# Optimization experiments

Hardware: AMD Instinct MI355X
Metric: run time of the kernel (lower is better)

Reference implementation:

```python
import jax, jax.numpy as jnp
import numpy as np

NUM_TRAIN = 256  # num_train_anchors
N, A, T = 8, 131072, 64


def _make_boxes(key, shape2):
    # shape2 = (..., 2) of (y, x); returns valid boxes (y1, x1, y2, x2) in [0, 1]
    k1, k2 = jax.random.split(key)
    c1 = jax.random.uniform(k1, shape2, dtype=jnp.float32)
    c2 = jax.random.uniform(k2, shape2, dtype=jnp.float32)
    lo = jnp.minimum(c1, c2)
    hi = jnp.maximum(c1, c2)
    return jnp.stack([lo[..., 0], lo[..., 1], hi[..., 0], hi[..., 1]], axis=-1)


def setup_inputs() -> dict:
    key = jax.random.key(0)
    ka, kt, kp, kn = jax.random.split(key, 4)
    return {
        "anchors": _make_boxes(ka, (N, A, 2)),
        "true_bboxes": _make_boxes(kt, (N, T, 2)),
        "rand_pos": jax.random.uniform(kp, (N, A), dtype=jnp.float32),
        "rand_neg": jax.random.uniform(kn, (N, A), dtype=jnp.float32),
    }


def _bbox_overlap(anchors, gt):
    # anchors [A,4], gt [T,4] -> IoU [A,T]
    ay1, ax1, ay2, ax2 = [anchors[:, i] for i in range(4)]
    gy1, gx1, gy2, gx2 = [gt[:, i] for i in range(4)]
    a_area = (ay2 - ay1) * (ax2 - ax1)                       # [A]
    g_area = (gy2 - gy1) * (gx2 - gx1)                       # [T]
    ih = jnp.clip(jnp.minimum(ay2[:, None], gy2[None, :]) - jnp.maximum(ay1[:, None], gy1[None, :]), 0.0)
    iw = jnp.clip(jnp.minimum(ax2[:, None], gx2[None, :]) - jnp.maximum(ax1[:, None], gx1[None, :]), 0.0)
    inter = ih * iw                                          # [A,T]
    union = a_area[:, None] + g_area[None, :] - inter
    return jnp.where(union > 0, inter / jnp.where(union > 0, union, 1.0), 0.0)


def _rank_of(scores):
    # rank[i] = position of element i in ascending sort of scores
    order = jnp.argsort(scores)
    return jnp.zeros(scores.shape[0], jnp.int32).at[order].set(jnp.arange(scores.shape[0], dtype=jnp.int32))


def _compute_bbox_deltas(anchors, gt):
    # standard (dy, dx, dh, dw) encoding with safe denominators
    ah = anchors[:, 2] - anchors[:, 0]
    aw = anchors[:, 3] - anchors[:, 1]
    acy = anchors[:, 0] + 0.5 * ah
    acx = anchors[:, 1] + 0.5 * aw
    gh = gt[:, 2] - gt[:, 0]
    gw = gt[:, 3] - gt[:, 1]
    gcy = gt[:, 0] + 0.5 * gh
    gcx = gt[:, 1] + 0.5 * gw
    ah_s = jnp.where(ah > 0, ah, 1.0)
    aw_s = jnp.where(aw > 0, aw, 1.0)
    gh_s = jnp.where(gh > 0, gh, 1.0)
    gw_s = jnp.where(gw > 0, gw, 1.0)
    return jnp.stack([(gcy - acy) / ah_s, (gcx - acx) / aw_s,
                      jnp.log(gh_s / ah_s), jnp.log(gw_s / aw_s)], axis=-1)


def _get_targets(anchors, gt, r_pos, r_neg):
    na = anchors.shape[0]
    # strip_out_of_bounds_anchors: zero out anchors falling outside [0,1]^2 (keeps static shape)
    inb = (anchors[:, 0] >= 0) & (anchors[:, 1] >= 0) & (anchors[:, 2] <= 1) & (anchors[:, 3] <= 1)
    anchors = jnp.where(inb[:, None], anchors, 0.0)

    overlaps = _bbox_overlap(anchors, gt)                    # [A,T]

    # --- class assignment ---
    iou_max_val = jnp.max(overlaps, axis=1)                  # [A]
    classes = jnp.full((na,), -1, jnp.int32)
    classes = jnp.where(iou_max_val < 0.3, 0, classes)
    iou_max_anchor = jnp.argmax(overlaps, axis=0)            # [T] best anchor per gt
    pos_anchor = jnp.zeros((na,), jnp.int32).at[iou_max_anchor].set(1)
    classes = jnp.where(pos_anchor > 0, 1, classes)
    classes = jnp.where(iou_max_val >= 0.7, 1, classes)

    # --- subsample positives to NUM_TRAIN//2 (uniform random subset) ---
    pos = classes > 0
    rank_p = _rank_of(jnp.where(pos, r_pos, jnp.inf))
    keep_pos = pos & (rank_p < NUM_TRAIN // 2)
    classes = jnp.where(pos & ~keep_pos, -1, classes)
    n_pos = jnp.sum(keep_pos.astype(jnp.int32))

    # --- subsample negatives to NUM_TRAIN - n_pos ---
    desired_neg = NUM_TRAIN - n_pos
    neg = classes == 0
    rank_n = _rank_of(jnp.where(neg, r_neg, jnp.inf))
    keep_neg = neg & (rank_n < desired_neg)
    classes = jnp.where(neg & ~keep_neg, -1, classes)

    # --- deltas for positive anchors ---
    best_gt = jnp.argmax(overlaps, axis=1)                   # [A]
    deltas = _compute_bbox_deltas(anchors, gt[best_gt])      # [A,4]
    deltas = jnp.where((classes > 0)[:, None], deltas, 0.0)
    return classes, deltas


def reference(anchors, true_bboxes, rand_pos, rand_neg):
    classes, deltas = jax.vmap(_get_targets)(anchors, true_bboxes, rand_pos, rand_neg)
    return classes, deltas
```

## Files before the change

kernel.cpp:

```cpp
#include <hip/hip_runtime.h>
#include <stdint.h>

#define N_B 8
#define A_N 131072
#define T_N 64
#define NUM_TRAIN 256
#define NEG_TAU 0.05f
#define ITEM_CAP 512
#define HSET 512
#define APT 4
#define SEG_A 1024
#define GBLK_A 128
#define CAPP 128
#define KB_THREADS 1024
#define BLK_C 128
#define SEG_C 1024

typedef unsigned long long u64;
typedef unsigned int u32;

__device__ __forceinline__ float iou_one(float ay1, float ax1, float ay2, float ax2,
                                         float a_area, float gy1, float gx1, float gy2,
                                         float gx2, float g_area) {
#pragma clang fp contract(off)
    float ih = fmaxf(fminf(ay2, gy2) - fmaxf(ay1, gy1), 0.0f);
    float iw = fmaxf(fminf(ax2, gx2) - fmaxf(ax1, gx1), 0.0f);
    float inter = ih * iw;
    float uni = (a_area + g_area) - inter;
    return uni > 0.0f ? inter / uni : 0.0f;
}

__global__ void __launch_bounds__(256) k_main(const float4* __restrict__ anchors4,
                                              const float4* __restrict__ gts4,
                                              const float* __restrict__ rpos,
                                              const float* __restrict__ rneg,
                                              unsigned char* __restrict__ preclass,
                                              long long* __restrict__ colpack,
                                              u64* __restrict__ pos_list,
                                              u64* __restrict__ neg_list,
                                              int* __restrict__ bcp, int* __restrict__ bcn,
                                              int* __restrict__ hist_pos,
                                              int* __restrict__ hist_neg) {
    __shared__ float4 gbox[T_N];
    __shared__ float gars[T_N];
    __shared__ u64 cmax[T_N];
    __shared__ int lcnt[2];
    int n = blockIdx.y, bx = blockIdx.x, tid = threadIdx.x, lane = tid & 63;
    int a0 = bx * SEG_A + tid;
    size_t nA = (size_t)n * A_N;

    if (tid < T_N) {
        float4 gb = gts4[n * T_N + tid];
        gbox[tid] = gb;
        {
#pragma clang fp contract(off)
            gars[tid] = (gb.z - gb.x) * (gb.w - gb.y);
        }
        cmax[tid] = 0;
    }
    if (tid < 2) lcnt[tid] = 0;
    __syncthreads();

    float ay1[APT], ax1[APT], ay2[APT], ax2[APT], aar[APT], vmax[APT];
#pragma unroll
    for (int k = 0; k < APT; k++) {
        float4 ab = anchors4[nA + a0 + k * 256];
        float y1 = ab.x, x1 = ab.y, y2 = ab.z, x2 = ab.w;
        bool inb = (y1 >= 0.f) && (x1 >= 0.f) && (y2 <= 1.f) && (x2 <= 1.f);
        if (!inb) { y1 = x1 = y2 = x2 = 0.f; }
        ay1[k] = y1; ax1[k] = x1; ay2[k] = y2; ax2[k] = x2;
        {
#pragma clang fp contract(off)
            aar[k] = (y2 - y1) * (x2 - x1);
        }
        vmax[k] = 0.f;
    }

#pragma unroll 4
    for (int jj = 0; jj < T_N; jj++) {
        int j = (lane + jj) & (T_N - 1);
        float4 gb = gbox[j];
        float gar = gars[j];
        float vb = iou_one(ay1[0], ax1[0], ay2[0], ax2[0], aar[0], gb.x, gb.y, gb.z, gb.w, gar);
        vmax[0] = fmaxf(vmax[0], vb);
        int kb = 0;
#pragma unroll
        for (int k = 1; k < APT; k++) {
            float v = iou_one(ay1[k], ax1[k], ay2[k], ax2[k], aar[k], gb.x, gb.y, gb.z, gb.w, gar);
            vmax[k] = fmaxf(vmax[k], v);
            if (v > vb) { vb = v; kb = k; }
        }
        u64 pk = ((u64)__float_as_uint(vb) << 32) | (u32)(~(u32)(a0 + (kb << 8)));
        atomicMax(&cmax[j], pk);
    }

    size_t segbase = ((size_t)(n * GBLK_A + bx)) << 7;
#pragma unroll
    for (int k = 0; k < APT; k++) {
        int a = a0 + k * 256;
        float vm = vmax[k];
        int c0 = (vm < 0.3f) ? 0 : ((vm >= 0.7f) ? 1 : -1);
        preclass[nA + a] = (unsigned char)(signed char)c0;
        if (c0 == 1) {
            int sl = atomicAdd(&lcnt[0], 1);
            if (sl < CAPP) {
                float r = rpos[nA + a];
                pos_list[segbase + sl] = ((u64)__float_as_uint(r) << 32) | (u32)a;
                int bb = (int)(r * 256.0f); bb = bb > 255 ? 255 : bb;
                atomicAdd(&hist_pos[(n << 8) + bb], 1);
            }
        } else if (c0 == 0) {
            float r = rneg[nA + a];
            if (r < NEG_TAU) {
                int sl = atomicAdd(&lcnt[1], 1);
                if (sl < CAPP) {
                    neg_list[segbase + sl] = ((u64)__float_as_uint(r) << 32) | (u32)a;
                    int bb = (int)(r * (256.0f / NEG_TAU)); bb = bb > 255 ? 255 : bb;
                    atomicAdd(&hist_neg[(n << 8) + bb], 1);
                }
            }
        }
    }
    __syncthreads();
    if (tid < T_N) atomicMax(&colpack[(n << 6) + tid], (long long)cmax[tid]);
    if (tid == 0) {
        bcp[n * GBLK_A + bx] = lcnt[0] < CAPP ? lcnt[0] : CAPP;
        bcn[n * GBLK_A + bx] = lcnt[1] < CAPP ? lcnt[1] : CAPP;
    }
}

__device__ __forceinline__ bool in_hset(const int* hset, int a) {
    u32 h = ((u32)a * 2654435761u) >> 23 & (HSET - 1);
    while (true) {
        int v = hset[h];
        if (v == -1) return false;
        if (v == a) return true;
        h = (h + 1) & (HSET - 1);
    }
}

__device__ u64 select_from_hist(const u64* lists, const int* cnts,
                                const u64* extras, int ecnt, const int* hset, bool use_excl,
                                int k, float scale, u64 ovf_all,
                                int* hist, u64* items, int* misc, int* wsum, u64* result) {
    int tid = threadIdx.x, lane = tid & 63, wid = tid >> 6;
    if (tid == 0) { misc[0] = 0; *result = ovf_all; }
    __syncthreads();

    int h = 0, v = 0;
    if (tid < 256) { h = hist[tid]; v = h; }
#pragma unroll
    for (int d = 1; d < 64; d <<= 1) {
        int t = __shfl_up(v, d, 64);
        if (lane >= d) v += t;
    }
    if (tid < 256 && lane == 63) wsum[wid] = v;
    __syncthreads();
    int total = wsum[0] + wsum[1] + wsum[2] + wsum[3];
    if (tid < 256) {
        int base = 0;
        for (int w = 0; w < wid; w++) base += wsum[w];
        int incl = base + v, exc = incl - h;
        if (k >= exc && k < incl) { misc[1] = tid; misc[2] = exc; }
    }
    __syncthreads();
    if (k >= total) return ovf_all;
    int b = misc[1], before = misc[2];

    int seg = tid & (GBLK_A - 1), part = tid >> 7;
    int c = cnts[seg];
    const ulonglong2* b2 = (const ulonglong2*)(lists + ((size_t)seg << 7));
    int nch = (c + 1) >> 1;
    for (int ci = part; ci < nch; ci += KB_THREADS / GBLK_A) {
        ulonglong2 q = b2[ci];
        {
            u64 p = q.x; int a = (int)(u32)p;
            if (!use_excl || !in_hset(hset, a)) {
                float vv = __uint_as_float((u32)(p >> 32));
                int bn = (int)(vv * scale); bn = bn > 255 ? 255 : bn;
                if (bn == b) { int ix = atomicAdd(&misc[0], 1); if (ix < ITEM_CAP) items[ix] = p; }
            }
        }
        if (2 * ci + 1 < c) {
            u64 p = q.y; int a = (int)(u32)p;
            if (!use_excl || !in_hset(hset, a)) {
                float vv = __uint_as_float((u32)(p >> 32));
                int bn = (int)(vv * scale); bn = bn > 255 ? 255 : bn;
                if (bn == b) { int ix = atomicAdd(&misc[0], 1); if (ix < ITEM_CAP) items[ix] = p; }
            }
        }
    }
    for (int i = tid; i < ecnt; i += KB_THREADS) {
        u64 p = extras[i];
        float vv = __uint_as_float((u32)(p >> 32));
        int bn = (int)(vv * scale); bn = bn > 255 ? 255 : bn;
        if (bn == b) { int ix = atomicAdd(&misc[0], 1); if (ix < ITEM_CAP) items[ix] = p; }
    }
    __syncthreads();
    int m = misc[0]; m = m < ITEM_CAP ? m : ITEM_CAP;
    int target = k - before;
    for (int i = tid; i < m; i += KB_THREADS) {
        u64 p = items[i];
        int r = 0;
        for (int j = 0; j < m; j++) r += (items[j] < p);
        if (r == target) *result = p;
    }
    __syncthreads();
    u64 res = *result;
    __syncthreads();
    return res;
}

__global__ void __launch_bounds__(KB_THREADS) k_B(const u64* __restrict__ pos_list,
                                                  const u64* __restrict__ neg_list,
                                                  const int* __restrict__ bcp,
                                                  const int* __restrict__ bcn,
                                                  const long long* __restrict__ colpack,
                                                  const unsigned char* __restrict__ preclass,
                                                  const float* __restrict__ rpos,
                                                  const float* __restrict__ rneg,
                                                  const int* __restrict__ hist_pos_g,
                                                  const int* __restrict__ hist_neg_g,
                                                  int* __restrict__ wnr_g,
                                                  u64* __restrict__ cutoff) {
    __shared__ int wnrs[T_N];
    __shared__ u64 extras[T_N];
    __shared__ int hist[256];
    __shared__ u64 items[ITEM_CAP];
    __shared__ int hset[HSET];
    __shared__ int misc[4];
    __shared__ int wsum[4];
    __shared__ int shr[4];
    __shared__ u64 result;
    int n = blockIdx.y, role = blockIdx.x, tid = threadIdx.x, lane = tid & 63;
    size_t nA = (size_t)n * A_N;

    if (tid < 256) hist[tid] = (role == 0 ? hist_pos_g : hist_neg_g)[(n << 8) + tid];
    if (tid == 0) shr[1] = 0;
    for (int i = tid; i < HSET; i += KB_THREADS) hset[i] = -1;
    __syncthreads();

    if (tid < T_N) {
        u64 m = (u64)colpack[(n << 6) + tid];
        int w = (int)(~(u32)(m & 0xFFFFFFFFull));
        wnrs[tid] = w;
        if (role == 0) wnr_g[n * T_N + tid] = w;
        u32 hh = ((u32)w * 2654435761u) >> 23 & (HSET - 1);
        while (true) {
            int old = atomicCAS(&hset[hh], -1, w);
            if (old == -1 || old == w) break;
            hh = (hh + 1) & (HSET - 1);
        }
    }
    if (role == 1) {
        int pv = (tid < 256) ? hist_pos_g[(n << 8) + tid] : 0;
#pragma unroll
        for (int off = 32; off > 0; off >>= 1) pv += __shfl_xor(pv, off, 64);
        if (lane == 0 && tid < 256) atomicAdd(&shr[1], pv);
    }
    __syncthreads();

    if (tid < T_N) {
        int w = wnrs[tid];
        bool dup = false;
        for (int t2 = 0; t2 < tid; t2++) dup |= (wnrs[t2] == w);
        int pc = (int)(signed char)preclass[nA + w];
        bool val = !dup && (pc != 1);
        u64 mask = __ballot(val);
        if (role == 0 && val) {
            int ix = (int)__popcll(mask & ((1ull << lane) - 1));
            extras[ix] = ((u64)__float_as_uint(rpos[nA + w]) << 32) | (u32)w;
        }
        if (role == 1 && !dup && pc == 0) {
            float r = rneg[nA + w];
            if (r < NEG_TAU) {
                int bb = (int)(r * (256.0f / NEG_TAU)); bb = bb > 255 ? 255 : bb;
                atomicAdd(&hist[bb], -1);
            }
        }
        if (tid == 0) shr[0] = (int)__popcll(mask);
    }
    __syncthreads();
    int extra_cnt = shr[0];

    if (role == 0) {
        for (int i = tid; i < extra_cnt; i += KB_THREADS) {
            float vv = __uint_as_float((u32)(extras[i] >> 32));
            int bb = (int)(vv * 256.0f); bb = bb > 255 ? 255 : bb;
            atomicAdd(&hist[bb], 1);
        }
        u64 cpos = select_from_hist(pos_list + (((size_t)n * GBLK_A) << 7), bcp + n * GBLK_A,
                                    extras, extra_cnt, hset, false,
                                    NUM_TRAIN / 2, 256.0f, ~0ull,
                                    hist, items, misc, wsum, &result);
        if (tid == 0) cutoff[2 * n] = cpos;
    } else {
        int P = shr[1] + extra_cnt;
        int n_pos = P < NUM_TRAIN / 2 ? P : NUM_TRAIN / 2;
        int k_neg = NUM_TRAIN - n_pos;
        u64 cneg = select_from_hist(neg_list + (((size_t)n * GBLK_A) << 7), bcn + n * GBLK_A,
                                    nullptr, 0, hset, true,
                                    k_neg, 256.0f / NEG_TAU, ((u64)__float_as_uint(NEG_TAU) << 32),
                                    hist, items, misc, wsum, &result);
        if (tid == 0) cutoff[2 * n + 1] = cneg;
    }
}

__global__ void __launch_bounds__(256) k_C(const float4* __restrict__ anchors4,
                                           const float4* __restrict__ gts4,
                                           const u32* __restrict__ preclass32,
                                           const int* __restrict__ wnr_g,
                                           const float4* __restrict__ rpos4,
                                           const float4* __restrict__ rneg4,
                                           const u64* __restrict__ cutoff,
                                           float4* __restrict__ out_classes4,
                                           float4* __restrict__ out_deltas) {
    __shared__ float4 gbox[T_N];
    __shared__ float gars[T_N];
    __shared__ u32 wbm[32];
    __shared__ u32 pbm[32];
    int n = blockIdx.y, bx = blockIdx.x, tid = threadIdx.x;
    size_t nA = (size_t)n * A_N;
    if (tid < 32) { wbm[tid] = 0; pbm[tid] = 0; }
    __syncthreads();
    if (tid < T_N) {
        float4 gb = gts4[n * T_N + tid];
        gbox[tid] = gb;
        {
#pragma clang fp contract(off)
            gars[tid] = (gb.z - gb.x) * (gb.w - gb.y);
        }
        int w = wnr_g[n * T_N + tid];
        int d = w - bx * SEG_C;
        if ((u32)d < (u32)SEG_C) atomicOr(&wbm[d >> 5], 1u << (d & 31));
    }
    __syncthreads();

    size_t gi4 = nA / 4 + bx * 256 + tid;
    u32 pcw = preclass32[gi4];
    float4 rp = rpos4[gi4];
    float4 rn = rneg4[gi4];
    float rpv[4] = {rp.x, rp.y, rp.z, rp.w};
    float rnv[4] = {rn.x, rn.y, rn.z, rn.w};
    int a0 = (bx * 256 + tid) * 4;
    u64 cp = cutoff[2 * n], cn = cutoff[2 * n + 1];

    u32 marked = (wbm[tid >> 3] >> ((tid & 7) * 4)) & 0xF;

    float fcv[4];
#pragma unroll
    for (int j = 0; j < 4; j++) {
        int c = (int)(signed char)((pcw >> (8 * j)) & 0xFF);
        if ((marked >> j) & 1) c = 1;
        int a = a0 + j;
        int fc = -1;
        if (c == 1) {
            u64 p = ((u64)__float_as_uint(rpv[j]) << 32) | (u32)a;
            fc = (p < cp) ? 1 : -1;
        } else if (c == 0) {
            u64 p = ((u64)__float_as_uint(rnv[j]) << 32) | (u32)a;
            fc = (p < cn) ? 0 : -1;
        }
        fcv[j] = (float)fc;
        if (fc == 1) {
            int s = 4 * tid + j;
            atomicOr(&pbm[s >> 5], 1u << (s & 31));
        }
    }
    out_classes4[gi4] = make_float4(fcv[0], fcv[1], fcv[2], fcv[3]);
    __syncthreads();

    int base = bx * SEG_C;
#pragma unroll
    for (int j = 0; j < 4; j++) {
        int s = j * 256 + tid;
        float4 d = make_float4(0.f, 0.f, 0.f, 0.f);
        if ((pbm[s >> 5] >> (s & 31)) & 1) {
            int a = base + s;
            float4 ab = anchors4[nA + a];
            float ay1 = ab.x, ax1 = ab.y, ay2 = ab.z, ax2 = ab.w;
            bool inb = (ay1 >= 0.f) && (ax1 >= 0.f) && (ay2 <= 1.f) && (ax2 <= 1.f);
            if (!inb) { ay1 = ax1 = ay2 = ax2 = 0.f; }
            float a_area;
            {
#pragma clang fp contract(off)
                a_area = (ay2 - ay1) * (ax2 - ax1);
            }
            float vm = 0.f; int jb = 0;
            for (int t = 0; t < T_N; t++) {
                float4 gb = gbox[t];
                float v = iou_one(ay1, ax1, ay2, ax2, a_area, gb.x, gb.y, gb.z, gb.w, gars[t]);
                bool g = v > vm;
                vm = g ? v : vm;
                jb = g ? t : jb;
            }
            float4 gb = gbox[jb];
            float ah = ay2 - ay1, aw = ax2 - ax1;
            float acy = ay1 + 0.5f * ah, acx = ax1 + 0.5f * aw;
            float gh = gb.z - gb.x, gw = gb.w - gb.y;
            float gcy = gb.x + 0.5f * gh, gcx = gb.y + 0.5f * gw;
            float ah_s = ah > 0.f ? ah : 1.f, aw_s = aw > 0.f ? aw : 1.f;
            float gh_s = gh > 0.f ? gh : 1.f, gw_s = gw > 0.f ? gw : 1.f;
            d.x = (gcy - acy) / ah_s;
            d.y = (gcx - acx) / aw_s;
            d.z = logf(gh_s / ah_s);
            d.w = logf(gw_s / aw_s);
        }
        out_deltas[nA + base + s] = d;
    }
}

extern "C" void kernel_launch(void* const* d_in, const int* in_sizes, int n_in,
                              void* d_out, int out_size, void* d_ws, size_t ws_size,
                              hipStream_t stream) {
    const float4* anchors4 = (const float4*)d_in[0];
    const float4* gts4     = (const float4*)d_in[1];
    const float*  rpos     = (const float*)d_in[2];
    const float*  rneg     = (const float*)d_in[3];

    char* p = (char*)d_ws;
    u64* cutoff   = (u64*)p;  p += 2 * N_B * sizeof(u64);
    long long* colpack = (long long*)p; p += N_B * T_N * sizeof(long long);
    u64* pos_list = (u64*)p;  p += (size_t)N_B * GBLK_A * CAPP * sizeof(u64);
    u64* neg_list = (u64*)p;  p += (size_t)N_B * GBLK_A * CAPP * sizeof(u64);
    unsigned char* preclass = (unsigned char*)p; p += (size_t)N_B * A_N;
    int* bcp  = (int*)p;  p += N_B * GBLK_A * sizeof(int);
    int* bcn  = (int*)p;  p += N_B * GBLK_A * sizeof(int);
    int* wnr  = (int*)p;  p += N_B * T_N * sizeof(int);
    int* hist_pos_g = (int*)p; p += N_B * 256 * sizeof(int);
    int* hist_neg_g = (int*)p; p += N_B * 256 * sizeof(int);

    float4* out_classes4 = (float4*)d_out;
    float4* out_deltas   = (float4*)((float*)d_out + (size_t)N_B * A_N);

    hipMemsetAsync(hist_pos_g, 0, 2 * N_B * 256 * sizeof(int), stream);

    k_main<<<dim3(GBLK_A, N_B), 256, 0, stream>>>(anchors4, gts4, rpos, rneg, preclass,
                                                  colpack, pos_list, neg_list, bcp, bcn,
                                                  hist_pos_g, hist_neg_g);
    k_B<<<dim3(2, N_B), KB_THREADS, 0, stream>>>(pos_list, neg_list, bcp, bcn, colpack,
                                                 preclass, rpos, rneg, hist_pos_g, hist_neg_g,
                                                 wnr, cutoff);
    k_C<<<dim3(BLK_C, N_B), 256, 0, stream>>>(anchors4, gts4, (const u32*)preclass, wnr,
                                              (const float4*)rpos, (const float4*)rneg,
                                              cutoff, out_classes4, out_deltas);
}
```

Measured before the change: 170.0 us.

## Fuse selection kernel into main kernel via last-block-done pattern

Removes the separate k_B launch. Each k_main block increments a per-image done counter, and the last block to finish runs the positive and then the negative threshold selection. The main grid is also resplit into twice as many blocks with two anchors per thread, and the counter is zeroed by the existing memset. This saves a kernel launch and gap, but the selection now runs serially in one 256-thread block per image instead of two 1024-thread blocks, and k_main carries more shared memory.

```diff
diff --git a/kernel.cpp b/kernel.cpp
--- a/kernel.cpp
+++ b/kernel.cpp
@@ -8,11 +8,10 @@
 #define NEG_TAU 0.05f
 #define ITEM_CAP 512
 #define HSET 512
-#define APT 4
-#define SEG_A 1024
-#define GBLK_A 128
+#define APT 2
+#define SEG_A 512
+#define GBLK_A 256
 #define CAPP 128
-#define KB_THREADS 1024
 #define BLK_C 128
 #define SEG_C 1024
 
@@ -30,6 +29,89 @@
     return uni > 0.0f ? inter / uni : 0.0f;
 }
 
+__device__ u64 tail_select(const u64* lists, const int* cnts,
+                           const u64* extras, int ecnt, const int* hset, bool use_excl,
+                           int k, float scale, u64 ovf_all,
+                           int* hist, u64* items, int* misc, int* wsum, u64* result) {
+    int tid = threadIdx.x, lane = tid & 63, wid = tid >> 6;
+    if (tid == 0) { misc[0] = 0; *result = ovf_all; }
+    __syncthreads();
+
+    int h = hist[tid], v = h;
+#pragma unroll
+    for (int d = 1; d < 64; d <<= 1) {
+        int t = __shfl_up(v, d, 64);
+        if (lane >= d) v += t;
+    }
+    if (lane == 63) wsum[wid] = v;
+    __syncthreads();
+    int total = wsum[0] + wsum[1] + wsum[2] + wsum[3];
+    int base = 0;
+    for (int w = 0; w < wid; w++) base += wsum[w];
+    int incl = base + v, exc = incl - h;
+    if (k >= exc && k < incl) { misc[1] = tid; misc[2] = exc; }
+    if (tid == 0) misc[3] = total;
+    __syncthreads();
+    if (k >= total) return ovf_all;
+    int b = misc[1], before = misc[2];
+
+    int c = cnts[tid];
+    const ulonglong2* b2 = (const ulonglong2*)(lists + ((size_t)tid << 7));
+    int nch = (c + 1) >> 1;
+    {
+        ulonglong2 q;
+        if (nch > 0) q = b2[0];
+        for (int ci = 0; ci < nch; ci++) {
+            ulonglong2 qn;
+            if (ci + 1 < nch) qn = b2[ci + 1];
+            {
+                u64 p = q.x; int a = (int)(u32)p;
+                if (!use_excl || ([&]{ u32 hh = ((u32)a * 2654435761u) >> 23 & (HSET - 1);
+                                       while (true) { int vv = hset[hh];
+                                           if (vv == -1) return true;
+                                           if (vv == a) return false;
+                                           hh = (hh + 1) & (HSET - 1); } }())) {
+                    float vv = __uint_as_float((u32)(p >> 32));
+                    int bn = (int)(vv * scale); bn = bn > 255 ? 255 : bn;
+                    if (bn == b) { int ix = atomicAdd(&misc[0], 1); if (ix < ITEM_CAP) items[ix] = p; }
+                }
+            }
+            if (2 * ci + 1 < c) {
+                u64 p = q.y; int a = (int)(u32)p;
+                if (!use_excl || ([&]{ u32 hh = ((u32)a * 2654435761u) >> 23 & (HSET - 1);
+                                       while (true) { int vv = hset[hh];
+                                           if (vv == -1) return true;
+                                           if (vv == a) return false;
+                                           hh = (hh + 1) & (HSET - 1); } }())) {
+                    float vv = __uint_as_float((u32)(p >> 32));
+                    int bn = (int)(vv * scale); bn = bn > 255 ? 255 : bn;
+                    if (bn == b) { int ix = atomicAdd(&misc[0], 1); if (ix < ITEM_CAP) items[ix] = p; }
+                }
+            }
+            q = qn;
+        }
+    }
+    for (int i = tid; i < ecnt; i += 256) {
+        u64 p = extras[i];
+        float vv = __uint_as_float((u32)(p >> 32));
+        int bn = (int)(vv * scale); bn = bn > 255 ? 255 : bn;
+        if (bn == b) { int ix = atomicAdd(&misc[0], 1); if (ix < ITEM_CAP) items[ix] = p; }
+    }
+    __syncthreads();
+    int m = misc[0]; m = m < ITEM_CAP ? m : ITEM_CAP;
+    int target = k - before;
+    for (int i = tid; i < m; i += 256) {
+        u64 p = items[i];
+        int r = 0;
+        for (int j = 0; j < m; j++) r += (items[j] < p);
+        if (r == target) *result = p;
+    }
+    __syncthreads();
+    u64 res = *result;
+    __syncthreads();
+    return res;
+}
+
 __global__ void __launch_bounds__(256) k_main(const float4* __restrict__ anchors4,
                                               const float4* __restrict__ gts4,
                                               const float* __restrict__ rpos,
@@ -40,11 +122,25 @@
                                               u64* __restrict__ neg_list,
                                               int* __restrict__ bcp, int* __restrict__ bcn,
                                               int* __restrict__ hist_pos,
-                                              int* __restrict__ hist_neg) {
+                                              int* __restrict__ hist_neg,
+                                              int* __restrict__ done_cnt,
+                                              int* __restrict__ wnr_g,
+                                              u64* __restrict__ cutoff) {
     __shared__ float4 gbox[T_N];
     __shared__ float gars[T_N];
     __shared__ u64 cmax[T_N];
     __shared__ int lcnt[2];
+    __shared__ int hist[256];
+    __shared__ u64 items[ITEM_CAP];
+    __shared__ int hset[HSET];
+    __shared__ u64 extras[T_N];
+    __shared__ int wnrs[T_N];
+    __shared__ int misc[4];
+    __shared__ int wsum[4];
+    __shared__ int shr[4];
+    __shared__ u64 result;
+    __shared__ int slast;
+
     int n = blockIdx.y, bx = blockIdx.x, tid = threadIdx.x, lane = tid & 63;
     int a0 = bx * SEG_A + tid;
     size_t nA = (size_t)n * A_N;
@@ -127,124 +223,25 @@
         bcp[n * GBLK_A + bx] = lcnt[0] < CAPP ? lcnt[0] : CAPP;
         bcn[n * GBLK_A + bx] = lcnt[1] < CAPP ? lcnt[1] : CAPP;
     }
-}
-
-__device__ __forceinline__ bool in_hset(const int* hset, int a) {
-    u32 h = ((u32)a * 2654435761u) >> 23 & (HSET - 1);
-    while (true) {
-        int v = hset[h];
-        if (v == -1) return false;
-        if (v == a) return true;
-        h = (h + 1) & (HSET - 1);
-    }
-}
-
-__device__ u64 select_from_hist(const u64* lists, const int* cnts,
-                                const u64* extras, int ecnt, const int* hset, bool use_excl,
-                                int k, float scale, u64 ovf_all,
-                                int* hist, u64* items, int* misc, int* wsum, u64* result) {
-    int tid = threadIdx.x, lane = tid & 63, wid = tid >> 6;
-    if (tid == 0) { misc[0] = 0; *result = ovf_all; }
-    __syncthreads();
-
-    int h = 0, v = 0;
-    if (tid < 256) { h = hist[tid]; v = h; }
-#pragma unroll
-    for (int d = 1; d < 64; d <<= 1) {
-        int t = __shfl_up(v, d, 64);
-        if (lane >= d) v += t;
-    }
-    if (tid < 256 && lane == 63) wsum[wid] = v;
-    __syncthreads();
-    int total = wsum[0] + wsum[1] + wsum[2] + wsum[3];
-    if (tid < 256) {
-        int base = 0;
-        for (int w = 0; w < wid; w++) base += wsum[w];
-        int incl = base + v, exc = incl - h;
-        if (k >= exc && k < incl) { misc[1] = tid; misc[2] = exc; }
-    }
-    __syncthreads();
-    if (k >= total) return ovf_all;
-    int b = misc[1], before = misc[2];
-
-    int seg = tid & (GBLK_A - 1), part = tid >> 7;
-    int c = cnts[seg];
-    const ulonglong2* b2 = (const ulonglong2*)(lists + ((size_t)seg << 7));
-    int nch = (c + 1) >> 1;
-    for (int ci = part; ci < nch; ci += KB_THREADS / GBLK_A) {
-        ulonglong2 q = b2[ci];
-        {
-            u64 p = q.x; int a = (int)(u32)p;
-            if (!use_excl || !in_hset(hset, a)) {
-                float vv = __uint_as_float((u32)(p >> 32));
-                int bn = (int)(vv * scale); bn = bn > 255 ? 255 : bn;
-                if (bn == b) { int ix = atomicAdd(&misc[0], 1); if (ix < ITEM_CAP) items[ix] = p; }
-            }
-        }
-        if (2 * ci + 1 < c) {
-            u64 p = q.y; int a = (int)(u32)p;
-            if (!use_excl || !in_hset(hset, a)) {
-                float vv = __uint_as_float((u32)(p >> 32));
-                int bn = (int)(vv * scale); bn = bn > 255 ? 255 : bn;
-                if (bn == b) { int ix = atomicAdd(&misc[0], 1); if (ix < ITEM_CAP) items[ix] = p; }
-            }
-        }
-    }
-    for (int i = tid; i < ecnt; i += KB_THREADS) {
-        u64 p = extras[i];
-        float vv = __uint_as_float((u32)(p >> 32));
-        int bn = (int)(vv * scale); bn = bn > 255 ? 255 : bn;
-        if (bn == b) { int ix = atomicAdd(&misc[0], 1); if (ix < ITEM_CAP) items[ix] = p; }
-    }
-    __syncthreads();
-    int m = misc[0]; m = m < ITEM_CAP ? m : ITEM_CAP;
-    int target = k - before;
-    for (int i = tid; i < m; i += KB_THREADS) {
-        u64 p = items[i];
-        int r = 0;
-        for (int j = 0; j < m; j++) r += (items[j] < p);
-        if (r == target) *result = p;
-    }
-    __syncthreads();
-    u64 res = *result;
-    __syncthreads();
-    return res;
-}
-
-__global__ void __launch_bounds__(KB_THREADS) k_B(const u64* __restrict__ pos_list,
-                                                  const u64* __restrict__ neg_list,
-                                                  const int* __restrict__ bcp,
-                                                  const int* __restrict__ bcn,
-                                                  const long long* __restrict__ colpack,
-                                                  const unsigned char* __restrict__ preclass,
-                                                  const float* __restrict__ rpos,
-                                                  const float* __restrict__ rneg,
-                                                  const int* __restrict__ hist_pos_g,
-                                                  const int* __restrict__ hist_neg_g,
-                                                  int* __restrict__ wnr_g,
-                                                  u64* __restrict__ cutoff) {
-    __shared__ int wnrs[T_N];
-    __shared__ u64 extras[T_N];
-    __shared__ int hist[256];
-    __shared__ u64 items[ITEM_CAP];
-    __shared__ int hset[HSET];
-    __shared__ int misc[4];
-    __shared__ int wsum[4];
-    __shared__ int shr[4];
-    __shared__ u64 result;
-    int n = blockIdx.y, role = blockIdx.x, tid = threadIdx.x, lane = tid & 63;
-    size_t nA = (size_t)n * A_N;
-
-    if (tid < 256) hist[tid] = (role == 0 ? hist_pos_g : hist_neg_g)[(n << 8) + tid];
-    if (tid == 0) shr[1] = 0;
-    for (int i = tid; i < HSET; i += KB_THREADS) hset[i] = -1;
-    __syncthreads();
-
+
+    __threadfence();
+    __syncthreads();
+    if (tid == 0) slast = (atomicAdd(&done_cnt[n], 1) == GBLK_A - 1) ? 1 : 0;
+    __syncthreads();
+    if (!slast) return;
+    __threadfence();
+
+    for (int i = tid; i < HSET; i += 256) hset[i] = -1;
+    hist[tid] = hist_pos[(n << 8) + tid];
+    __syncthreads();
+
+    int w = 0, pcv = 0;
+    bool dup = false;
     if (tid < T_N) {
         u64 m = (u64)colpack[(n << 6) + tid];
-        int w = (int)(~(u32)(m & 0xFFFFFFFFull));
+        w = (int)(~(u32)(m & 0xFFFFFFFFull));
         wnrs[tid] = w;
-        if (role == 0) wnr_g[n * T_N + tid] = w;
+        wnr_g[n * T_N + tid] = w;
         u32 hh = ((u32)w * 2654435761u) >> 23 & (HSET - 1);
         while (true) {
             int old = atomicCAS(&hset[hh], -1, w);
@@ -252,58 +249,51 @@
             hh = (hh + 1) & (HSET - 1);
         }
     }
-    if (role == 1) {
-        int pv = (tid < 256) ? hist_pos_g[(n << 8) + tid] : 0;
-#pragma unroll
-        for (int off = 32; off > 0; off >>= 1) pv += __shfl_xor(pv, off, 64);
-        if (lane == 0 && tid < 256) atomicAdd(&shr[1], pv);
-    }
-    __syncthreads();
-
+    __syncthreads();
     if (tid < T_N) {
-        int w = wnrs[tid];
-        bool dup = false;
         for (int t2 = 0; t2 < tid; t2++) dup |= (wnrs[t2] == w);
-        int pc = (int)(signed char)preclass[nA + w];
-        bool val = !dup && (pc != 1);
+        pcv = (int)(signed char)preclass[nA + w];
+        bool val = !dup && (pcv != 1);
         u64 mask = __ballot(val);
-        if (role == 0 && val) {
-            int ix = (int)__popcll(mask & ((1ull << lane) - 1));
+        if (val) {
+            int ix = (int)__popcll(mask & ((1ull << tid) - 1));
             extras[ix] = ((u64)__float_as_uint(rpos[nA + w]) << 32) | (u32)w;
         }
-        if (role == 1 && !dup && pc == 0) {
-            float r = rneg[nA + w];
-            if (r < NEG_TAU) {
-                int bb = (int)(r * (256.0f / NEG_TAU)); bb = bb > 255 ? 255 : bb;
-                atomicAdd(&hist[bb], -1);
-            }
-        }
         if (tid == 0) shr[0] = (int)__popcll(mask);
     }
     __syncthreads();
     int extra_cnt = shr[0];
-
-    if (role == 0) {
-        for (int i = tid; i < extra_cnt; i += KB_THREADS) {
-            float vv = __uint_as_float((u32)(extras[i] >> 32));
-            int bb = (int)(vv * 256.0f); bb = bb > 255 ? 255 : bb;
-            atomicAdd(&hist[bb], 1);
-        }
-        u64 cpos = select_from_hist(pos_list + (((size_t)n * GBLK_A) << 7), bcp + n * GBLK_A,
-                                    extras, extra_cnt, hset, false,
-                                    NUM_TRAIN / 2, 256.0f, ~0ull,
-                                    hist, items, misc, wsum, &result);
-        if (tid == 0) cutoff[2 * n] = cpos;
-    } else {
-        int P = shr[1] + extra_cnt;
-        int n_pos = P < NUM_TRAIN / 2 ? P : NUM_TRAIN / 2;
-        int k_neg = NUM_TRAIN - n_pos;
-        u64 cneg = select_from_hist(neg_list + (((size_t)n * GBLK_A) << 7), bcn + n * GBLK_A,
-                                    nullptr, 0, hset, true,
-                                    k_neg, 256.0f / NEG_TAU, ((u64)__float_as_uint(NEG_TAU) << 32),
-                                    hist, items, misc, wsum, &result);
-        if (tid == 0) cutoff[2 * n + 1] = cneg;
-    }
+    for (int i = tid; i < extra_cnt; i += 256) {
+        float vv = __uint_as_float((u32)(extras[i] >> 32));
+        int bb = (int)(vv * 256.0f); bb = bb > 255 ? 255 : bb;
+        atomicAdd(&hist[bb], 1);
+    }
+    __syncthreads();
+
+    u64 cpos = tail_select(pos_list + (((size_t)n * GBLK_A) << 7), bcp + n * GBLK_A,
+                           extras, extra_cnt, hset, false,
+                           NUM_TRAIN / 2, 256.0f, ~0ull,
+                           hist, items, misc, wsum, &result);
+    int P = misc[3];
+    if (tid == 0) cutoff[2 * n] = cpos;
+
+    hist[tid] = hist_neg[(n << 8) + tid];
+    __syncthreads();
+    if (tid < T_N && !dup && pcv == 0) {
+        float r = rneg[nA + w];
+        if (r < NEG_TAU) {
+            int bb = (int)(r * (256.0f / NEG_TAU)); bb = bb > 255 ? 255 : bb;
+            atomicAdd(&hist[bb], -1);
+        }
+    }
+    __syncthreads();
+    int n_pos = P < NUM_TRAIN / 2 ? P : NUM_TRAIN / 2;
+    u64 cneg = tail_select(neg_list + (((size_t)n * GBLK_A) << 7), bcn + n * GBLK_A,
+                           nullptr, 0, hset, true,
+                           NUM_TRAIN - n_pos, 256.0f / NEG_TAU,
+                           ((u64)__float_as_uint(NEG_TAU) << 32),
+                           hist, items, misc, wsum, &result);
+    if (tid == 0) cutoff[2 * n + 1] = cneg;
 }
 
 __global__ void __launch_bounds__(256) k_C(const float4* __restrict__ anchors4,
@@ -429,18 +419,17 @@
     int* wnr  = (int*)p;  p += N_B * T_N * sizeof(int);
     int* hist_pos_g = (int*)p; p += N_B * 256 * sizeof(int);
     int* hist_neg_g = (int*)p; p += N_B * 256 * sizeof(int);
+    int* done_cnt   = (int*)p; p += N_B * sizeof(int);
 
     float4* out_classes4 = (float4*)d_out;
     float4* out_deltas   = (float4*)((float*)d_out + (size_t)N_B * A_N);
 
-    hipMemsetAsync(hist_pos_g, 0, 2 * N_B * 256 * sizeof(int), stream);
+    hipMemsetAsync(hist_pos_g, 0, (2 * N_B * 256 + N_B) * sizeof(int), stream);
 
     k_main<<<dim3(GBLK_A, N_B), 256, 0, stream>>>(anchors4, gts4, rpos, rneg, preclass,
                                                   colpack, pos_list, neg_list, bcp, bcn,
-                                                  hist_pos_g, hist_neg_g);
-    k_B<<<dim3(2, N_B), KB_THREADS, 0, stream>>>(pos_list, neg_list, bcp, bcn, colpack,
-                                                 preclass, rpos, rneg, hist_pos_g, hist_neg_g,
-                                                 wnr, cutoff);
+                                                  hist_pos_g, hist_neg_g, done_cnt,
+                                                  wnr, cutoff);
     k_C<<<dim3(BLK_C, N_B), 256, 0, stream>>>(anchors4, gts4, (const u32*)preclass, wnr,
                                               (const float4*)rpos, (const float4*)rneg,
                                               cutoff, out_classes4, out_deltas);
```

Result: slower. 304.7 us (+79.2%).
